# Kernel tuning notes

Measured on AMD Instinct MI355X. Metric: run time of the kernel, lower is better.

## Reference

```python
import jax, jax.numpy as jnp
import numpy as np

N = 50000      # nodes in batched graph
E = 800000     # edges
IN_DIM = 16
HID = 64
NH = 4         # heads
G = 128        # graphs in batch
OUT_DIM = 32
NUM_LAYERS = 8
NEG_SLOPE = 0.2  # DGL GATv2Conv default


def setup_inputs() -> dict:
    key = jax.random.key(0)
    ks = jax.random.split(key, 12)
    feat = jax.random.normal(ks[0], (N, IN_DIM), dtype=jnp.float32)
    src = jax.random.randint(ks[1], (E,), 0, N, dtype=jnp.int32)
    dst = jax.random.randint(ks[2], (E,), 0, N, dtype=jnp.int32)
    graph_ids = jnp.sort(jax.random.randint(ks[3], (N,), 0, G, dtype=jnp.int32))
    is_root = jax.random.randint(ks[4], (N,), 0, 2, dtype=jnp.int32)
    s_in = 1.0 / np.sqrt(IN_DIM)
    s_h = 1.0 / np.sqrt(2 * HID)
    s_o = 1.0 / np.sqrt(HID)
    return {
        'feat': feat, 'src': src, 'dst': dst,
        'graph_ids': graph_ids, 'is_root': is_root,
        'W_in': jax.random.normal(ks[5], (IN_DIM, HID), jnp.float32) * s_in,
        'b_in': jnp.zeros((HID,), jnp.float32),
        'W_src': jax.random.normal(ks[6], (2 * HID, NH * HID), jnp.float32) * s_h,
        'b_src': jnp.zeros((NH * HID,), jnp.float32),
        'W_dst': jax.random.normal(ks[7], (2 * HID, NH * HID), jnp.float32) * s_h,
        'b_dst': jnp.zeros((NH * HID,), jnp.float32),
        'attn': jax.random.normal(ks[8], (NH, HID), jnp.float32) * s_o,
        'W_out': jax.random.normal(ks[9], (HID, OUT_DIM), jnp.float32) * s_o,
        'b_out': jnp.zeros((OUT_DIM,), jnp.float32),
    }


def reference(feat, src, dst, graph_ids, is_root,
              W_in, b_in, W_src, b_src, W_dst, b_dst, attn, W_out, b_out):
    h0 = feat @ W_in + b_in                       # [N, HID]
    h = h0
    for _ in range(NUM_LAYERS):
        x = jnp.concatenate([h, h0], axis=1)      # [N, 2*HID]
        fs = (x @ W_src + b_src).reshape(-1, NH, HID)  # [N, NH, HID]
        fd = (x @ W_dst + b_dst).reshape(-1, NH, HID)
        # per-edge GATv2 attention logits
        e = jax.nn.leaky_relu(fs[src] + fd[dst], NEG_SLOPE)   # [E, NH, HID]
        s = jnp.einsum('ehd,hd->eh', e, attn)                 # [E, NH]
        # segment softmax over incoming edges of each dst node
        m = jax.ops.segment_max(s, dst, num_segments=N)       # [N, NH]
        a = jnp.exp(s - m[dst])
        denom = jax.ops.segment_sum(a, dst, num_segments=N)
        alpha = a / denom[dst]                                # [E, NH]
        # weighted aggregation of source features
        agg = jax.ops.segment_sum(alpha[:, :, None] * fs[src], dst,
                                  num_segments=N)             # [N, NH, HID]
        h = jnp.tanh(agg).sum(axis=1)                         # [N, HID]
    # root-weighted readout per graph
    hg = jax.ops.segment_sum(h * is_root.astype(h.dtype)[:, None],
                             graph_ids, num_segments=G)       # [G, HID]
    return hg @ W_out + b_out                                 # [G, OUT_DIM]
```

## Files before the change

### kernel.cpp

```cpp
#include <hip/hip_runtime.h>
#include <math.h>

#define N_NODES 50000
#define N_EDGES 800000
#define IN_DIM  16
#define HID     64
#define NH      4
#define NGRAPH  128
#define OUT_DIM 32
#define NUM_LAYERS 8
#define NEG_SLOPE 0.2f

#define SCAN_BLOCKS ((N_NODES + 255) / 256)

typedef unsigned short u16;
typedef unsigned char  u8;
typedef _Float16 h2   __attribute__((ext_vector_type(2)));
typedef _Float16 f16x8 __attribute__((ext_vector_type(8)));
typedef float f32x2 __attribute__((ext_vector_type(2)));
typedef __attribute__((ext_vector_type(4))) float f32x4;

static __device__ __forceinline__ u16 f2h(float f) {
    _Float16 h = (_Float16)f; u16 r; __builtin_memcpy(&r, &h, 2); return r;
}
static __device__ __forceinline__ float h2f_lo(unsigned w) {
    _Float16 h; u16 u = (u16)w; __builtin_memcpy(&h, &u, 2); return (float)h;
}
static __device__ __forceinline__ h2 shfl_h2(h2 v, int mask) {
    int i; __builtin_memcpy(&i, &v, 4); i = __shfl_xor(i, mask);
    h2 r; __builtin_memcpy(&r, &i, 4); return r;
}
static __device__ __forceinline__ h2 bcast_h2(float f) {
    _Float16 h = (_Float16)f; h2 r; r[0] = h; r[1] = h; return r;
}
static __device__ __forceinline__ h2 pkrtz_h2(float a, float b) {
    auto v = __builtin_amdgcn_cvt_pkrtz(a, b);
    h2 r; __builtin_memcpy(&r, &v, 4); return r;
}

#define DPP_XOR1(x) __uint_as_float((unsigned)__builtin_amdgcn_update_dpp(0, (int)__float_as_uint(x), 0xB1, 0xF, 0xF, true))
#define DPP_XOR2(x) __uint_as_float((unsigned)__builtin_amdgcn_update_dpp(0, (int)__float_as_uint(x), 0x4E, 0xF, 0xF, true))


__global__ void k_build_wpack(const float* __restrict__ Wsrc, const float* __restrict__ bsrc,
                              const float* __restrict__ Wdst, const float* __restrict__ bdst,
                              const float* __restrict__ attn,
                              u16* __restrict__ Wpack, float* __restrict__ bcat,
                              u16* __restrict__ an_h) {
    int tid = blockIdx.x * 256 + threadIdx.x;
    int i = tid & 7;
    int l = (tid >> 3) & 63;
    int rest = tid >> 9;
    int kt = rest & 3;
    int nt = rest >> 2;
    int k = kt * 32 + (l >> 4) * 8 + i;
    int col = nt * 16 + (l & 15);
    float v = (col < 256) ? Wsrc[k * 256 + col] : Wdst[k * 256 + (col - 256)];
    Wpack[tid] = f2h(v);
    if (tid < 512) bcat[tid] = (tid < 256) ? bsrc[tid] : bdst[tid - 256];
    if (tid < 256) an_h[tid] = f2h(attn[tid] * 1.44269504f);
}

__global__ void k_hist(const int* __restrict__ dst, int* __restrict__ deg) {
    int e = blockIdx.x * 256 + threadIdx.x;
    if (e < N_EDGES) atomicAdd(&deg[dst[e]], 1);
}

__global__ void k_blocksum(const int* __restrict__ deg, int* __restrict__ bsum) {
    __shared__ int sm[256];
    int i = blockIdx.x * 256 + threadIdx.x;
    sm[threadIdx.x] = (i < N_NODES) ? deg[i] : 0;
    __syncthreads();
    for (int s = 128; s > 0; s >>= 1) {
        if (threadIdx.x < s) sm[threadIdx.x] += sm[threadIdx.x + s];
        __syncthreads();
    }
    if (threadIdx.x == 0) bsum[blockIdx.x] = sm[0];
}

__global__ void k_scanbsum(int* __restrict__ bsum) {
    __shared__ int sm[256];
    int t = threadIdx.x;
    int v = (t < SCAN_BLOCKS) ? bsum[t] : 0;
    sm[t] = v;
    __syncthreads();
    for (int s = 1; s < 256; s <<= 1) {
        int x = (t >= s) ? sm[t - s] : 0;
        __syncthreads();
        sm[t] += x;
        __syncthreads();
    }
    if (t < SCAN_BLOCKS) bsum[t] = sm[t] - v;
}

__global__ void k_rowptr(const int* __restrict__ deg, const int* __restrict__ bsum,
                         int* __restrict__ row_ptr) {
    __shared__ int sm[256];
    int i = blockIdx.x * 256 + threadIdx.x;
    int v = (i < N_NODES) ? deg[i] : 0;
    sm[threadIdx.x] = v;
    __syncthreads();
    for (int s = 1; s < 256; s <<= 1) {
        int t = (threadIdx.x >= (unsigned)s) ? sm[threadIdx.x - s] : 0;
        __syncthreads();
        sm[threadIdx.x] += t;
        __syncthreads();
    }
    if (i < N_NODES) row_ptr[i] = bsum[blockIdx.x] + sm[threadIdx.x] - v;
}

__global__ void k_scatter(const int* __restrict__ src, const int* __restrict__ dst,
                          const int* __restrict__ row_ptr, int* __restrict__ cursor,
                          int* __restrict__ csr_src) {
    int e = blockIdx.x * 256 + threadIdx.x;
    if (e < N_EDGES) {
        int d = dst[e];
        int pos = atomicAdd(&cursor[d], 1);
        csr_src[row_ptr[d] + pos] = src[e];
    }
}

__global__ __launch_bounds__(256) void k_in_gemm(const float* __restrict__ feat,
                                                 const float* __restrict__ W,
                                                 const float* __restrict__ b,
                                                 u16* __restrict__ h0h) {
    __shared__ float sW[IN_DIM * HID];
    __shared__ float sb[HID];
    int t = threadIdx.x;
    for (int i = t; i < IN_DIM * HID; i += 256) sW[i] = W[i];
    if (t < HID) sb[t] = b[t];
    __syncthreads();
    int wid = (blockIdx.x * 256 + t) >> 6;
    int lane = t & 63;
    const float* f = feat + wid * IN_DIM;
    float acc = sb[lane];
    #pragma unroll
    for (int k = 0; k < IN_DIM; k++) acc += f[k] * sW[k * HID + lane];
    h0h[wid * HID + lane] = f2h(acc);
}


#define ST_STRIDE 152
__global__ __launch_bounds__(256) void k_gemm_mfma(const u16* __restrict__ hb,
                                                   const u16* __restrict__ h0b,
                                                   const u16* __restrict__ Wpack,
                                                   const float* __restrict__ bcat,
                                                   u8* __restrict__ fs8,
                                                   u16* __restrict__ fdh) {
    __shared__ u16 sStage[4][2432];
    int tid = threadIdx.x;
    int g  = blockIdx.x & 3;
    int tb = blockIdx.x >> 2;
    int l = tid & 63, w = tid >> 6;
    int lr = l & 15, lg = l >> 4;
    const u16* WpG = Wpack + g * 16384;

    size_t row0 = (size_t)(tb * 4 + w) * 16;
    if (row0 >= N_NODES) return;

    f32x4 acc[8];
    #pragma unroll
    for (int nt = 0; nt < 8; nt++) acc[nt] = (f32x4){0.f, 0.f, 0.f, 0.f};

    #pragma unroll
    for (int kt = 0; kt < 4; kt++) {
        const u16* A = (kt < 2) ? hb : h0b;
        f16x8 a = *(const f16x8*)(A + (row0 + lr) * HID + (kt & 1) * 32 + lg * 8);
        #pragma unroll
        for (int nt = 0; nt < 8; nt++) {
            f16x8 bfr = *(const f16x8*)(WpG + nt * 2048 + kt * 512 + l * 8);
            acc[nt] = __builtin_amdgcn_mfma_f32_16x16x32_f16(a, bfr, acc[nt], 0, 0, 0);
        }
    }

    u16* myst = sStage[w];
    #pragma unroll
    for (int nt = 0; nt < 8; nt++) {
        float bv = bcat[g * 128 + nt * 16 + lr];
        #pragma unroll
        for (int j = 0; j < 4; j++)
            myst[(lg * 4 + j) * ST_STRIDE + nt * 16 + lr] = f2h(acc[nt][j] + bv);
    }
    #pragma unroll
    for (int j = 0; j < 4; j++) {
        int rloc = j * 4 + lg;
        f16x8 v = *(const f16x8*)(myst + rloc * ST_STRIDE + lr * 8);
        if (g < 2) {
            int p0 = __builtin_amdgcn_cvt_pk_fp8_f32((float)v[0], (float)v[1], 0, false);
            int p1 = __builtin_amdgcn_cvt_pk_fp8_f32((float)v[2], (float)v[3], 0, false);
            int p2 = __builtin_amdgcn_cvt_pk_fp8_f32((float)v[4], (float)v[5], 0, false);
            int p3 = __builtin_amdgcn_cvt_pk_fp8_f32((float)v[6], (float)v[7], 0, false);
            uint2 o8;
            o8.x = (unsigned)(p0 & 0xffff) | ((unsigned)p1 << 16);
            o8.y = (unsigned)(p2 & 0xffff) | ((unsigned)p3 << 16);
            *(uint2*)(fs8 + (row0 + rloc) * 256 + g * 128 + lr * 8) = o8;
        } else {
            *(f16x8*)(fdh + (row0 + rloc) * 256 + (g - 2) * 128 + lr * 8) = v;
        }
    }
}

__global__ __launch_bounds__(256) void k_edge(const u8* __restrict__ fs8,
                                              const u16* __restrict__ fdh,
                                              const u16* __restrict__ an_h,
                                              const int* __restrict__ row_ptr,
                                              const int* __restrict__ deg,
                                              const int* __restrict__ csr_src,
                                              u16* __restrict__ h) {
    int wid = (blockIdx.x * 256 + threadIdx.x) >> 6;
    int lane = threadIdx.x & 63;
    int g  = lane >> 4;
    int ll = lane & 15;
    const size_t ebase = (size_t)ll * 16;

    h2 an[8], fdhv[8];
    {
        const uint4* ap = (const uint4*)(an_h + ebase);
        uint4 a0 = ap[0], a1 = ap[1];
        unsigned aw[8] = {a0.x, a0.y, a0.z, a0.w, a1.x, a1.y, a1.z, a1.w};
        __builtin_memcpy(an, aw, 32);
        const uint4* fp = (const uint4*)(fdh + (size_t)wid * 256 + ebase);
        uint4 b0 = fp[0], b1 = fp[1];
        unsigned fw[8] = {b0.x, b0.y, b0.z, b0.w, b1.x, b1.y, b1.z, b1.w};
        __builtin_memcpy(fdhv, fw, 32);
    }
    const h2 slope2 = {(_Float16)NEG_SLOPE, (_Float16)NEG_SLOPE};

    float m = -3.0e38f, denom = 0.f;
    h2 agg[8];
    #pragma unroll
    for (int q = 0; q < 8; q++) agg[q] = (h2){(_Float16)0.f, (_Float16)0.f};

    int r0 = row_ptr[wid], dg = deg[wid];
    for (int i = g; i < dg; i += 4) {
        int s = csr_src[r0 + i];
        uint4 A = *(const uint4*)(fs8 + (size_t)s * 256 + ebase);

        h2 f[8];
        {
            unsigned d[4] = {A.x, A.y, A.z, A.w};
            #pragma unroll
            for (int q = 0; q < 4; q++) {
                f32x2 lo = __builtin_amdgcn_cvt_pk_f32_fp8((int)d[q], false);
                f32x2 hi = __builtin_amdgcn_cvt_pk_f32_fp8((int)d[q], true);
                f[2*q]   = pkrtz_h2(lo[0], lo[1]);
                f[2*q+1] = pkrtz_h2(hi[0], hi[1]);
            }
        }
        float p0 = 0.f, p1 = 0.f;
        #pragma unroll
        for (int q = 0; q < 8; q += 2) {
            h2 e0 = f[q]   + fdhv[q];
            h2 e1 = f[q+1] + fdhv[q+1];
            h2 l0 = __builtin_elementwise_max(e0, e0 * slope2);
            h2 l1 = __builtin_elementwise_max(e1, e1 * slope2);
            p0 = __builtin_amdgcn_fdot2(l0, an[q],   p0, false);
            p1 = __builtin_amdgcn_fdot2(l1, an[q+1], p1, false);
        }
        float p = p0 + p1;
        p += DPP_XOR1(p);
        p += DPP_XOR2(p);

        float c;
        if (__builtin_expect(p > m + 4.f, 0)) {
            float rs = exp2f(m - p);
            h2 rs2 = bcast_h2(rs);
            #pragma unroll
            for (int q = 0; q < 8; q++) agg[q] = agg[q] * rs2;
            denom *= rs;
            m = p;
            c = 1.f;
        } else {
            c = exp2f(p - m);
        }
        h2 c2 = bcast_h2(c);
        #pragma unroll
        for (int q = 0; q < 8; q++) agg[q] = agg[q] + f[q] * c2;
        denom += c;
    }

    {
        float mm = fmaxf(m, __shfl_xor(m, 16));
        mm = fmaxf(mm, __shfl_xor(mm, 32));
        float sc = exp2f(m - mm);
        denom *= sc;
        h2 sc2 = bcast_h2(sc);
        #pragma unroll
        for (int q = 0; q < 8; q++) agg[q] = agg[q] * sc2;
        denom += __shfl_xor(denom, 16);
        denom += __shfl_xor(denom, 32);
        #pragma unroll
        for (int q = 0; q < 8; q++) {
            agg[q] = agg[q] + shfl_h2(agg[q], 16);
            agg[q] = agg[q] + shfl_h2(agg[q], 32);
        }
    }

    float inv = denom > 0.f ? __builtin_amdgcn_rcpf(denom) : 0.f;
    float inv2 = inv * 2.885390082f;

    h2 x0 = (g & 2) ? ((g & 1) ? agg[6] : agg[4]) : ((g & 1) ? agg[2] : agg[0]);
    h2 x1 = (g & 2) ? ((g & 1) ? agg[7] : agg[5]) : ((g & 1) ? agg[3] : agg[1]);
    float t[4] = {(float)x0[0], (float)x0[1], (float)x1[0], (float)x1[1]};
    #pragma unroll
    for (int j = 0; j < 4; j++) {
        float E = exp2f(t[j] * inv2);
        float r = __builtin_amdgcn_rcpf(E + 1.f);
        float v = fmaf(-2.f, r, 1.f);
        v += __shfl_xor(v, 4);
        v += __shfl_xor(v, 8);
        t[j] = v;
    }
    if (ll < 4) {
        uint2 o;
        o.x = (unsigned)f2h(t[0]) | ((unsigned)f2h(t[1]) << 16);
        o.y = (unsigned)f2h(t[2]) | ((unsigned)f2h(t[3]) << 16);
        *(uint2*)(h + (size_t)wid * 64 + ll * 16 + g * 4) = o;
    }
}


__global__ __launch_bounds__(256) void k_readout(const u16* __restrict__ h,
                                                 const int* __restrict__ graph_ids,
                                                 const int* __restrict__ is_root,
                                                 float* __restrict__ hg) {
    int wid = (blockIdx.x * 256 + threadIdx.x) >> 6;
    int lane = threadIdx.x & 63;
    if (is_root[wid]) {
        int g = graph_ids[wid];
        atomicAdd(&hg[g * HID + lane], h2f_lo(h[(size_t)wid * HID + lane]));
    }
}

__global__ void k_out_gemm(const float* __restrict__ hg, const float* __restrict__ W,
                           const float* __restrict__ b, float* __restrict__ out) {
    int i = blockIdx.x * 256 + threadIdx.x;
    if (i >= NGRAPH * OUT_DIM) return;
    int g = i >> 5, o = i & 31;
    float acc = b[o];
    #pragma unroll
    for (int k = 0; k < HID; k++) acc += hg[g * HID + k] * W[k * OUT_DIM + o];
    out[i] = acc;
}


extern "C" void kernel_launch(void* const* d_in, const int* in_sizes, int n_in,
                              void* d_out, int out_size, void* d_ws, size_t ws_size,
                              hipStream_t stream) {
    const float* feat      = (const float*)d_in[0];
    const int*   src       = (const int*)d_in[1];
    const int*   dst       = (const int*)d_in[2];
    const int*   graph_ids = (const int*)d_in[3];
    const int*   is_root   = (const int*)d_in[4];
    const float* W_in      = (const float*)d_in[5];
    const float* b_in      = (const float*)d_in[6];
    const float* W_src     = (const float*)d_in[7];
    const float* b_src     = (const float*)d_in[8];
    const float* W_dst     = (const float*)d_in[9];
    const float* b_dst     = (const float*)d_in[10];
    const float* attn      = (const float*)d_in[11];
    const float* W_out     = (const float*)d_in[12];
    const float* b_out     = (const float*)d_in[13];
    float* out = (float*)d_out;

    char* base = (char*)d_ws;
    size_t off = 0;
    auto carve = [&](size_t bytes) -> char* {
        char* p = base + off;
        off = (off + bytes + 255) & ~(size_t)255;
        return p;
    };
    u16*   h0b     = (u16*)carve((size_t)N_NODES * HID * 2);
    u16*   hb      = (u16*)carve((size_t)N_NODES * HID * 2);
    u8*    fs8     = (u8*)carve((size_t)N_NODES * 256);
    u16*   fdh     = (u16*)carve((size_t)N_NODES * 256 * 2);
    u16*   Wpack   = (u16*)carve(128 * 512 * 2);
    float* bcat    = (float*)carve(512 * 4);
    u16*   an_h    = (u16*)carve(256 * 2);
    int*   csr_src = (int*)carve((size_t)N_EDGES * 4);
    int*   row_ptr = (int*)carve((size_t)N_NODES * 4);
    int*   bsum    = (int*)carve(SCAN_BLOCKS * 4);
    char*  zero0   = carve(0);
    int*   deg     = (int*)carve((size_t)N_NODES * 4);
    int*   cursor  = (int*)carve((size_t)N_NODES * 4);
    float* hg      = (float*)carve((size_t)NGRAPH * HID * 4);
    char*  zero1   = base + off;
    if (off > ws_size) return;

    (void)hipMemsetAsync(zero0, 0, (size_t)(zero1 - zero0), stream);

    k_build_wpack<<<256, 256, 0, stream>>>(W_src, b_src, W_dst, b_dst, attn, Wpack, bcat, an_h);
    k_hist<<<(N_EDGES + 255) / 256, 256, 0, stream>>>(dst, deg);
    k_blocksum<<<SCAN_BLOCKS, 256, 0, stream>>>(deg, bsum);
    k_scanbsum<<<1, 256, 0, stream>>>(bsum);
    k_rowptr<<<SCAN_BLOCKS, 256, 0, stream>>>(deg, bsum, row_ptr);
    k_scatter<<<(N_EDGES + 255) / 256, 256, 0, stream>>>(src, dst, row_ptr, cursor, csr_src);

    k_in_gemm<<<N_NODES / 4, 256, 0, stream>>>(feat, W_in, b_in, h0b);

    const int gemm_grid = ((N_NODES / 16 + 3) / 4) * 4;
    for (int layer = 0; layer < NUM_LAYERS; layer++) {
        const u16* hcur = (layer == 0) ? h0b : hb;
        k_gemm_mfma<<<gemm_grid, 256, 0, stream>>>(hcur, h0b, Wpack, bcat, fs8, fdh);
        k_edge<<<N_NODES / 4, 256, 0, stream>>>(fs8, fdh, an_h, row_ptr, deg, csr_src, hb);
    }

    k_readout<<<N_NODES / 4, 256, 0, stream>>>(hb, graph_ids, is_root, hg);
    k_out_gemm<<<(NGRAPH * OUT_DIM + 255) / 256, 256, 0, stream>>>(hg, W_out, b_out, out);
}
```

Measured before the change: 844.3 us.

## Store node features in MFMA-fragment packed layout and compute two row tiles per wave

Node hidden states (h0 and h) are now stored in a tiled layout that matches the MFMA A-fragment order, so the GEMM reads each fragment as one contiguous 16-byte load per lane instead of strided row reads. Each wave now computes two 16-row tiles, reusing every loaded weight fragment across both. The edge kernel writes directly into the packed layout and is split into two launches over halves of the nodes. This raises register pressure in the GEMM and adds a kernel launch per layer. The split edge launch appears to have no benefit beyond an extra dispatch.

```diff
diff --git a/kernel.cpp b/kernel.cpp
--- a/kernel.cpp
+++ b/kernel.cpp
@@ -12,6 +12,7 @@
 #define NEG_SLOPE 0.2f
 
 #define SCAN_BLOCKS ((N_NODES + 255) / 256)
+#define NTILES (N_NODES / 16)
 
 typedef unsigned short u16;
 typedef unsigned char  u8;
@@ -36,6 +37,11 @@
 static __device__ __forceinline__ h2 pkrtz_h2(float a, float b) {
     auto v = __builtin_amdgcn_cvt_pkrtz(a, b);
     h2 r; __builtin_memcpy(&r, &v, 4); return r;
+}
+
+static __device__ __forceinline__ size_t pk_addr(int node, int d) {
+    return (size_t)(node >> 4) * 1024 + (size_t)((d >> 5) * 512 +
+           (((d & 31) >> 3) * 16 + (node & 15)) * 8 + (d & 7));
 }
 
 #define DPP_XOR1(x) __uint_as_float((unsigned)__builtin_amdgcn_update_dpp(0, (int)__float_as_uint(x), 0xB1, 0xF, 0xF, true))
@@ -123,7 +129,7 @@
 __global__ __launch_bounds__(256) void k_in_gemm(const float* __restrict__ feat,
                                                  const float* __restrict__ W,
                                                  const float* __restrict__ b,
-                                                 u16* __restrict__ h0h) {
+                                                 u16* __restrict__ h0p) {
     __shared__ float sW[IN_DIM * HID];
     __shared__ float sb[HID];
     int t = threadIdx.x;
@@ -136,13 +142,13 @@
     float acc = sb[lane];
     #pragma unroll
     for (int k = 0; k < IN_DIM; k++) acc += f[k] * sW[k * HID + lane];
-    h0h[wid * HID + lane] = f2h(acc);
+    h0p[pk_addr(wid, lane)] = f2h(acc);
 }
 
 
 #define ST_STRIDE 152
-__global__ __launch_bounds__(256) void k_gemm_mfma(const u16* __restrict__ hb,
-                                                   const u16* __restrict__ h0b,
+__global__ __launch_bounds__(256) void k_gemm_mfma(const u16* __restrict__ hbp,
+                                                   const u16* __restrict__ h0p,
                                                    const u16* __restrict__ Wpack,
                                                    const float* __restrict__ bcat,
                                                    u8* __restrict__ fs8,
@@ -155,47 +161,59 @@
     int lr = l & 15, lg = l >> 4;
     const u16* WpG = Wpack + g * 16384;
 
-    size_t row0 = (size_t)(tb * 4 + w) * 16;
-    if (row0 >= N_NODES) return;
-
-    f32x4 acc[8];
-    #pragma unroll
-    for (int nt = 0; nt < 8; nt++) acc[nt] = (f32x4){0.f, 0.f, 0.f, 0.f};
+    int t0 = tb * 8 + w * 2;
+    if (t0 >= NTILES) return;
+    bool has1 = (t0 + 1) < NTILES;
+
+    f32x4 acc[2][8];
+    #pragma unroll
+    for (int rt = 0; rt < 2; rt++)
+        #pragma unroll
+        for (int nt = 0; nt < 8; nt++) acc[rt][nt] = (f32x4){0.f, 0.f, 0.f, 0.f};
 
     #pragma unroll
     for (int kt = 0; kt < 4; kt++) {
-        const u16* A = (kt < 2) ? hb : h0b;
-        f16x8 a = *(const f16x8*)(A + (row0 + lr) * HID + (kt & 1) * 32 + lg * 8);
+        const u16* Ap = (kt < 2) ? hbp : h0p;
+        int hf = kt & 1;
+        f16x8 a0 = *(const f16x8*)(Ap + (size_t)t0 * 1024 + hf * 512 + l * 8);
+        f16x8 a1 = has1 ? *(const f16x8*)(Ap + (size_t)(t0 + 1) * 1024 + hf * 512 + l * 8) : a0;
         #pragma unroll
         for (int nt = 0; nt < 8; nt++) {
             f16x8 bfr = *(const f16x8*)(WpG + nt * 2048 + kt * 512 + l * 8);
-            acc[nt] = __builtin_amdgcn_mfma_f32_16x16x32_f16(a, bfr, acc[nt], 0, 0, 0);
+            acc[0][nt] = __builtin_amdgcn_mfma_f32_16x16x32_f16(a0, bfr, acc[0][nt], 0, 0, 0);
+            acc[1][nt] = __builtin_amdgcn_mfma_f32_16x16x32_f16(a1, bfr, acc[1][nt], 0, 0, 0);
         }
     }
 
     u16* myst = sStage[w];
     #pragma unroll
-    for (int nt = 0; nt < 8; nt++) {
-        float bv = bcat[g * 128 + nt * 16 + lr];
-        #pragma unroll
-        for (int j = 0; j < 4; j++)
-            myst[(lg * 4 + j) * ST_STRIDE + nt * 16 + lr] = f2h(acc[nt][j] + bv);
-    }
-    #pragma unroll
-    for (int j = 0; j < 4; j++) {
-        int rloc = j * 4 + lg;
-        f16x8 v = *(const f16x8*)(myst + rloc * ST_STRIDE + lr * 8);
-        if (g < 2) {
-            int p0 = __builtin_amdgcn_cvt_pk_fp8_f32((float)v[0], (float)v[1], 0, false);
-            int p1 = __builtin_amdgcn_cvt_pk_fp8_f32((float)v[2], (float)v[3], 0, false);
-            int p2 = __builtin_amdgcn_cvt_pk_fp8_f32((float)v[4], (float)v[5], 0, false);
-            int p3 = __builtin_amdgcn_cvt_pk_fp8_f32((float)v[6], (float)v[7], 0, false);
-            uint2 o8;
-            o8.x = (unsigned)(p0 & 0xffff) | ((unsigned)p1 << 16);
-            o8.y = (unsigned)(p2 & 0xffff) | ((unsigned)p3 << 16);
-            *(uint2*)(fs8 + (row0 + rloc) * 256 + g * 128 + lr * 8) = o8;
-        } else {
-            *(f16x8*)(fdh + (row0 + rloc) * 256 + (g - 2) * 128 + lr * 8) = v;
+    for (int rt = 0; rt < 2; rt++) {
+        int t = t0 + rt;
+        if (t >= NTILES) break;
+        size_t row0 = (size_t)t * 16;
+        #pragma unroll
+        for (int nt = 0; nt < 8; nt++) {
+            float bv = bcat[g * 128 + nt * 16 + lr];
+            #pragma unroll
+            for (int j = 0; j < 4; j++)
+                myst[(lg * 4 + j) * ST_STRIDE + nt * 16 + lr] = f2h(acc[rt][nt][j] + bv);
+        }
+        #pragma unroll
+        for (int j = 0; j < 4; j++) {
+            int rloc = j * 4 + lg;
+            f16x8 v = *(const f16x8*)(myst + rloc * ST_STRIDE + lr * 8);
+            if (g < 2) {
+                int p0 = __builtin_amdgcn_cvt_pk_fp8_f32((float)v[0], (float)v[1], 0, false);
+                int p1 = __builtin_amdgcn_cvt_pk_fp8_f32((float)v[2], (float)v[3], 0, false);
+                int p2 = __builtin_amdgcn_cvt_pk_fp8_f32((float)v[4], (float)v[5], 0, false);
+                int p3 = __builtin_amdgcn_cvt_pk_fp8_f32((float)v[6], (float)v[7], 0, false);
+                uint2 o8;
+                o8.x = (unsigned)(p0 & 0xffff) | ((unsigned)p1 << 16);
+                o8.y = (unsigned)(p2 & 0xffff) | ((unsigned)p3 << 16);
+                *(uint2*)(fs8 + (row0 + rloc) * 256 + g * 128 + lr * 8) = o8;
+            } else {
+                *(f16x8*)(fdh + (row0 + rloc) * 256 + (g - 2) * 128 + lr * 8) = v;
+            }
         }
     }
 }
@@ -206,8 +224,8 @@
                                               const int* __restrict__ row_ptr,
                                               const int* __restrict__ deg,
                                               const int* __restrict__ csr_src,
-                                              u16* __restrict__ h) {
-    int wid = (blockIdx.x * 256 + threadIdx.x) >> 6;
+                                              u16* __restrict__ hbp, int base) {
+    int wid = base + ((blockIdx.x * 256 + threadIdx.x) >> 6);
     int lane = threadIdx.x & 63;
     int g  = lane >> 4;
     int ll = lane & 15;
@@ -312,15 +330,19 @@
         t[j] = v;
     }
     if (ll < 4) {
+        int half = ll >> 1;
+        int lg2 = (ll & 1) * 2 + (g >> 1);
+        size_t addr = (size_t)(wid >> 4) * 1024 + half * 512 +
+                      (lg2 * 16 + (wid & 15)) * 8 + (g & 1) * 4;
         uint2 o;
         o.x = (unsigned)f2h(t[0]) | ((unsigned)f2h(t[1]) << 16);
         o.y = (unsigned)f2h(t[2]) | ((unsigned)f2h(t[3]) << 16);
-        *(uint2*)(h + (size_t)wid * 64 + ll * 16 + g * 4) = o;
-    }
-}
-
-
-__global__ __launch_bounds__(256) void k_readout(const u16* __restrict__ h,
+        *(uint2*)(hbp + addr) = o;
+    }
+}
+
+
+__global__ __launch_bounds__(256) void k_readout(const u16* __restrict__ hbp,
                                                  const int* __restrict__ graph_ids,
                                                  const int* __restrict__ is_root,
                                                  float* __restrict__ hg) {
@@ -328,7 +350,7 @@
     int lane = threadIdx.x & 63;
     if (is_root[wid]) {
         int g = graph_ids[wid];
-        atomicAdd(&hg[g * HID + lane], h2f_lo(h[(size_t)wid * HID + lane]));
+        atomicAdd(&hg[g * HID + lane], h2f_lo(hbp[pk_addr(wid, lane)]));
     }
 }
 
@@ -370,8 +392,8 @@
         off = (off + bytes + 255) & ~(size_t)255;
         return p;
     };
-    u16*   h0b     = (u16*)carve((size_t)N_NODES * HID * 2);
-    u16*   hb      = (u16*)carve((size_t)N_NODES * HID * 2);
+    u16*   h0p     = (u16*)carve((size_t)N_NODES * HID * 2);
+    u16*   hbp     = (u16*)carve((size_t)N_NODES * HID * 2);
     u8*    fs8     = (u8*)carve((size_t)N_NODES * 256);
     u16*   fdh     = (u16*)carve((size_t)N_NODES * 256 * 2);
     u16*   Wpack   = (u16*)carve(128 * 512 * 2);
@@ -396,15 +418,17 @@
     k_rowptr<<<SCAN_BLOCKS, 256, 0, stream>>>(deg, bsum, row_ptr);
     k_scatter<<<(N_EDGES + 255) / 256, 256, 0, stream>>>(src, dst, row_ptr, cursor, csr_src);
 
-    k_in_gemm<<<N_NODES / 4, 256, 0, stream>>>(feat, W_in, b_in, h0b);
-
-    const int gemm_grid = ((N_NODES / 16 + 3) / 4) * 4;
+    k_in_gemm<<<N_NODES / 4, 256, 0, stream>>>(feat, W_in, b_in, h0p);
+
+    const int gemm_grid = ((NTILES + 7) / 8) * 4;
+    const int edge_grid = (N_NODES / 2) / 4;
     for (int layer = 0; layer < NUM_LAYERS; layer++) {
-        const u16* hcur = (layer == 0) ? h0b : hb;
-        k_gemm_mfma<<<gemm_grid, 256, 0, stream>>>(hcur, h0b, Wpack, bcat, fs8, fdh);
-        k_edge<<<N_NODES / 4, 256, 0, stream>>>(fs8, fdh, an_h, row_ptr, deg, csr_src, hb);
-    }
-
-    k_readout<<<N_NODES / 4, 256, 0, stream>>>(hb, graph_ids, is_root, hg);
+        const u16* hcur = (layer == 0) ? h0p : hbp;
+        k_gemm_mfma<<<gemm_grid, 256, 0, stream>>>(hcur, h0p, Wpack, bcat, fs8, fdh);
+        k_edge<<<edge_grid, 256, 0, stream>>>(fs8, fdh, an_h, row_ptr, deg, csr_src, hbp, 0);
+        k_edge<<<edge_grid, 256, 0, stream>>>(fs8, fdh, an_h, row_ptr, deg, csr_src, hbp, N_NODES / 2);
+    }
+
+    k_readout<<<N_NODES / 4, 256, 0, stream>>>(hbp, graph_ids, is_root, hg);
     k_out_gemm<<<(NGRAPH * OUT_DIM + 255) / 256, 256, 0, stream>>>(hg, W_out, b_out, out);
 }
```

After: 903.1 us. 7.0% more time.
